# Optimization experiments

Hardware: AMD Instinct MI355X
Metric: run time of the kernel (lower is better)

## Reference

```python
import jax, jax.numpy as jnp
import numpy as np

N_EMBED = 1024
HEAD_SIZE = 128
B, T = 4, 2048

def setup_inputs() -> dict:
    key = jax.random.key(0)
    kx, kq, kk, kv = jax.random.split(key, 4)
    bound = 1.0 / np.sqrt(N_EMBED)  # torch Linear default init range
    x = jax.random.normal(kx, (B, T, N_EMBED), dtype=jnp.float32)
    Wq = jax.random.uniform(kq, (N_EMBED, HEAD_SIZE), jnp.float32, -bound, bound)
    Wk = jax.random.uniform(kk, (N_EMBED, HEAD_SIZE), jnp.float32, -bound, bound)
    Wv = jax.random.uniform(kv, (N_EMBED, HEAD_SIZE), jnp.float32, -bound, bound)
    return {"x": x, "Wq": Wq, "Wk": Wk, "Wv": Wv}

def reference(x, Wq, Wk, Wv):
    Bn, Tn, C = x.shape
    q = x @ Wq  # [B,T,H]
    k = x @ Wk
    v = x @ Wv
    # NOTE: original scales by C**-0.5 where C = n_embed (not head_size)
    scale = C ** (-0.5)
    wei = jnp.einsum('bqh,bkh->bqk', q, k) * scale  # [B,T,T]
    causal = jnp.tril(jnp.ones((Tn, Tn), dtype=bool))
    wei = jnp.where(causal, wei, -jnp.inf)
    wei = jax.nn.softmax(wei, axis=-1)
    # dropout p=0.0 -> identity
    return jnp.einsum('bqk,bkh->bqh', wei, v)
```

## Files before the change

kernel.cpp:

```cpp
#include <hip/hip_runtime.h>
#include <stdint.h>

#define B_ 4
#define T_ 2048
#define C_ 1024
#define H_ 128
#define NEG_BIG -3.0e38f

typedef __attribute__((ext_vector_type(8))) short short8;
typedef __attribute__((ext_vector_type(4))) float f32x4;
typedef __attribute__((ext_vector_type(4))) unsigned short ushort4v;
typedef __attribute__((ext_vector_type(8))) unsigned short ushort8v;

__device__ __forceinline__ unsigned short f2bf(float f) {
  union { float f; unsigned u; } cv; cv.f = f;
  unsigned u = cv.u;
  return (unsigned short)((u + 0x7fffu + ((u >> 16) & 1u)) >> 16);
}

__device__ __forceinline__ float bf2f(unsigned short s) {
  union { unsigned u; float f; } cv; cv.u = ((unsigned)s) << 16;
  return cv.f;
}

__device__ __forceinline__ void gld16(const unsigned short* g, unsigned short* l) {
  __builtin_amdgcn_global_load_lds(
      (const __attribute__((address_space(1))) unsigned int*)g,
      (__attribute__((address_space(3))) unsigned int*)l, 16, 0, 0);
}

#define CSCALE 0.045084220027780106f

__global__ __launch_bounds__(256) void prep(const float* __restrict__ x,
                                            const float* __restrict__ Wq,
                                            const float* __restrict__ Wk,
                                            const float* __restrict__ Wv,
                                            unsigned short* __restrict__ xb,
                                            unsigned short* __restrict__ WbT) {
  if (blockIdx.x < 8192) {
    const int base = (blockIdx.x * 256 + threadIdx.x) * 4;
    f32x4 v = *(const f32x4*)(x + base);
    ushort4v p;
    p[0] = f2bf(v[0]); p[1] = f2bf(v[1]); p[2] = f2bf(v[2]); p[3] = f2bf(v[3]);
    *(ushort4v*)(xb + base) = p;
  } else {
    const int i = (blockIdx.x - 8192) * 256 + threadIdx.x;
    const int linear = i * 4;
    const int j = linear >> 10;
    const int k0 = linear & 1023;
    const float* W = (j < 128) ? Wq : (j < 256) ? Wk : Wv;
    const int h = j & 127;
    ushort4v p;
    p[0] = f2bf(W[(k0 + 0) * 128 + h]);
    p[1] = f2bf(W[(k0 + 1) * 128 + h]);
    p[2] = f2bf(W[(k0 + 2) * 128 + h]);
    p[3] = f2bf(W[(k0 + 3) * 128 + h]);
    *(ushort4v*)(WbT + linear) = p;
  }
}

__global__ __launch_bounds__(256) void qkv_proj(const unsigned short* __restrict__ xb,
                                                const unsigned short* __restrict__ WbT,
                                                unsigned short* __restrict__ Qb,
                                                unsigned short* __restrict__ Kb,
                                                unsigned short* __restrict__ VT) {
  __shared__ unsigned short As[2][64 * 64];
  __shared__ unsigned short Bs[2][96 * 64];

  const int tid  = threadIdx.x;
  const int wave = tid >> 6, lane = tid & 63;
  const int quad = lane >> 4, l15 = lane & 15;
  const int rb = blockIdx.x >> 2, cb = blockIdx.x & 3;
  const int gm0 = rb * 64, gn0 = cb * 96;
  const int wm = wave >> 1, wn = wave & 1;

  const int srow = lane >> 3, sslot = lane & 7;

  int aoff[2][2], boff[3][2];
#pragma unroll
  for (int mt = 0; mt < 2; ++mt) {
    const int r = wm * 32 + mt * 16 + l15;
#pragma unroll
    for (int ks = 0; ks < 2; ++ks)
      aoff[mt][ks] = r * 64 + (((ks * 4 + quad) ^ r) & 7) * 8;
  }
#pragma unroll
  for (int nt = 0; nt < 3; ++nt) {
    const int r = wn * 48 + nt * 16 + l15;
#pragma unroll
    for (int ks = 0; ks < 2; ++ks)
      boff[nt][ks] = r * 64 + (((ks * 4 + quad) ^ r) & 7) * 8;
  }

  f32x4 acc[2][3];
  const f32x4 zero4 = {0.f, 0.f, 0.f, 0.f};
#pragma unroll
  for (int mt = 0; mt < 2; ++mt)
#pragma unroll
    for (int nt = 0; nt < 3; ++nt) acc[mt][nt] = zero4;

#define STAGE_QKV(buf, kb_)                                                        \
  {                                                                                \
    const int ko = (kb_) * 64;                                                     \
    _Pragma("unroll")                                                              \
    for (int q = 0; q < 2; ++q) {                                                  \
      const int row = wave * 16 + q * 8 + srow;                                    \
      gld16(xb + (size_t)(gm0 + row) * C_ + ko + ((sslot ^ row) & 7) * 8,          \
            &As[buf][(wave * 16 + q * 8) * 64]);                                   \
    }                                                                              \
    _Pragma("unroll")                                                              \
    for (int q = 0; q < 3; ++q) {                                                  \
      const int row = wave * 24 + q * 8 + srow;                                    \
      gld16(WbT + (size_t)(gn0 + row) * C_ + ko + ((sslot ^ row) & 7) * 8,         \
            &Bs[buf][(wave * 24 + q * 8) * 64]);                                   \
    }                                                                              \
  }

  STAGE_QKV(0, 0);

  for (int kb = 0; kb < 16; ++kb) {
    __syncthreads();
    if (kb + 1 < 16) STAGE_QKV((kb + 1) & 1, kb + 1);
    const unsigned short* Ac = As[kb & 1];
    const unsigned short* Bc = Bs[kb & 1];
#pragma unroll
    for (int ks = 0; ks < 2; ++ks) {
      short8 a0 = *(const short8*)(Ac + aoff[0][ks]);
      short8 a1 = *(const short8*)(Ac + aoff[1][ks]);
      short8 b0 = *(const short8*)(Bc + boff[0][ks]);
      short8 b1 = *(const short8*)(Bc + boff[1][ks]);
      short8 b2 = *(const short8*)(Bc + boff[2][ks]);
      acc[0][0] = __builtin_amdgcn_mfma_f32_16x16x32_bf16(a0, b0, acc[0][0], 0, 0, 0);
      acc[0][1] = __builtin_amdgcn_mfma_f32_16x16x32_bf16(a0, b1, acc[0][1], 0, 0, 0);
      acc[0][2] = __builtin_amdgcn_mfma_f32_16x16x32_bf16(a0, b2, acc[0][2], 0, 0, 0);
      acc[1][0] = __builtin_amdgcn_mfma_f32_16x16x32_bf16(a1, b0, acc[1][0], 0, 0, 0);
      acc[1][1] = __builtin_amdgcn_mfma_f32_16x16x32_bf16(a1, b1, acc[1][1], 0, 0, 0);
      acc[1][2] = __builtin_amdgcn_mfma_f32_16x16x32_bf16(a1, b2, acc[1][2], 0, 0, 0);
    }
  }
#undef STAGE_QKV

#pragma unroll
  for (int mt = 0; mt < 2; ++mt) {
    const int row0 = gm0 + wm * 32 + mt * 16 + quad * 4;
#pragma unroll
    for (int nt = 0; nt < 3; ++nt) {
      const int colbase = gn0 + wn * 48 + nt * 16;
      const int col = colbase + l15;
      if (colbase < 128) {
#pragma unroll
        for (int r = 0; r < 4; ++r)
          Qb[(size_t)(row0 + r) * H_ + col] = f2bf(acc[mt][nt][r] * CSCALE);
      } else if (colbase < 256) {
#pragma unroll
        for (int r = 0; r < 4; ++r)
          Kb[(size_t)(row0 + r) * H_ + (col - 128)] = f2bf(acc[mt][nt][r]);
      } else {
        const int h = col - 256;
        const int bidx = row0 >> 11;
        const int t0 = row0 & 2047;
        ushort4v pk;
        pk[0] = f2bf(acc[mt][nt][0]); pk[1] = f2bf(acc[mt][nt][1]);
        pk[2] = f2bf(acc[mt][nt][2]); pk[3] = f2bf(acc[mt][nt][3]);
        *(ushort4v*)(VT + (size_t)(bidx * H_ + h) * T_ + t0) = pk;
      }
    }
  }
}

__global__ __launch_bounds__(256, 2) void attn1(const unsigned short* __restrict__ Qb,
                                                const unsigned short* __restrict__ Kb,
                                                const unsigned short* __restrict__ VT,
                                                unsigned short* __restrict__ Opart,
                                                float* __restrict__ mpart,
                                                float* __restrict__ lpart,
                                                float* __restrict__ out) {
  __shared__ unsigned short Ks[2][64 * 128];
  __shared__ unsigned short Vs[2][128 * 64];
  __shared__ unsigned short Pls[4][16 * 72];
  __shared__ float Als[4][16];

  const int bid = blockIdx.x;
  const int b  = bid & 3;
  const int j  = (bid >> 2) & 31;
  const int ch = bid >> 7;
  if (ch * 4 > j) return;
  const int ntiles = min(4, j + 1 - ch * 4);

  const int tid  = threadIdx.x;
  const int wave = tid >> 6, lane = tid & 63;
  const int quad = lane >> 4, l15 = lane & 15;

  const unsigned short* qrow = Qb + (size_t)(b * T_ + j * 64 + wave * 16 + l15) * H_;
  short8 aq[4];
#pragma unroll
  for (int ks = 0; ks < 4; ++ks)
    aq[ks] = *(const short8*)(qrow + ks * 32 + quad * 8);

  const unsigned short* Kb_b = Kb + (size_t)(b * T_) * H_;
  const unsigned short* VT_b = VT + (size_t)(b * H_) * T_;

  const int k_row4 = lane >> 4, k_slot = lane & 15;
  const int v_row8 = lane >> 3, v_slot = lane & 7;

#define STAGE_KV(buf, kv0_)                                                        \
  {                                                                                \
    _Pragma("unroll")                                                              \
    for (int i = 0; i < 4; ++i) {                                                  \
      const int r = wave * 16 + i * 4 + k_row4;                                    \
      const int c2 = (k_slot & 8) | ((k_slot ^ r) & 7);                            \
      gld16(Kb_b + (size_t)((kv0_) + r) * H_ + c2 * 8,                             \
            &Ks[buf][(wave * 16 + i * 4) * 128]);                                  \
    }                                                                              \
    _Pragma("unroll")                                                              \
    for (int i = 0; i < 4; ++i) {                                                  \
      const int h = wave * 32 + i * 8 + v_row8;                                    \
      gld16(VT_b + (size_t)h * T_ + (kv0_) + ((v_slot ^ h) & 7) * 8,               \
            &Vs[buf][(wave * 32 + i * 8) * 64]);                                   \
    }                                                                              \
  }

  STAGE_KV(0, ch * 256);

  const f32x4 zero4 = {0.f, 0.f, 0.f, 0.f};
  f32x4 O[8];
#pragma unroll
  for (int nth = 0; nth < 8; ++nth) O[nth] = zero4;
  float m_ = NEG_BIG, l_ = 0.f;

  for (int t = 0; t < ntiles; ++t) {
    __syncthreads();
    const int kv0 = ch * 256 + t * 64;
    if (t + 1 < ntiles) STAGE_KV((t + 1) & 1, kv0 + 64);

    const unsigned short* kb = Ks[t & 1];
    f32x4 ST[4];
    ST[0] = zero4; ST[1] = zero4; ST[2] = zero4; ST[3] = zero4;
#pragma unroll
    for (int ntl = 0; ntl < 4; ++ntl) {
      const int kvr = ntl * 16 + l15;
#pragma unroll
      for (int ks = 0; ks < 4; ++ks) {
        const int c = ks * 4 + quad;
        const int slot = (c & 8) | ((c ^ kvr) & 7);
        short8 kf = *(const short8*)(kb + kvr * 128 + slot * 8);
        ST[ntl] = __builtin_amdgcn_mfma_f32_16x16x32_bf16(kf, aq[ks], ST[ntl], 0, 0, 0);
      }
    }

    if (ch * 4 + t == j) {
      const int ql = j * 64 + wave * 16 + l15;
#pragma unroll
      for (int ntl = 0; ntl < 4; ++ntl)
#pragma unroll
        for (int r = 0; r < 4; ++r) {
          const int kl = kv0 + ntl * 16 + quad * 4 + r;
          if (kl > ql) ST[ntl][r] = NEG_BIG;
        }
    }

    float vmax = ST[0][0];
#pragma unroll
    for (int ntl = 0; ntl < 4; ++ntl)
#pragma unroll
      for (int r = 0; r < 4; ++r) vmax = fmaxf(vmax, ST[ntl][r]);
    vmax = fmaxf(vmax, __shfl_xor(vmax, 16));
    vmax = fmaxf(vmax, __shfl_xor(vmax, 32));
    const float mn = fmaxf(m_, vmax);
    const float alpha = __builtin_amdgcn_exp2f(m_ - mn);
    m_ = mn;
    float s = 0.f;
#pragma unroll
    for (int ntl = 0; ntl < 4; ++ntl)
#pragma unroll
      for (int r = 0; r < 4; ++r) {
        const float p = __builtin_amdgcn_exp2f(ST[ntl][r] - mn);
        ST[ntl][r] = p;
        s += p;
      }
    s += __shfl_xor(s, 16);
    s += __shfl_xor(s, 32);
    l_ = l_ * alpha + s;

#pragma unroll
    for (int ntl = 0; ntl < 4; ++ntl) {
      ushort4v pk;
      pk[0] = f2bf(ST[ntl][0]); pk[1] = f2bf(ST[ntl][1]);
      pk[2] = f2bf(ST[ntl][2]); pk[3] = f2bf(ST[ntl][3]);
      *(ushort4v*)(&Pls[wave][l15 * 72 + ntl * 16 + quad * 4]) = pk;
    }

    if (lane < 16) Als[wave][lane] = alpha;
    if (!__all(alpha == 1.f)) {
      f32x4 al4 = *(const f32x4*)&Als[wave][quad * 4];
#pragma unroll
      for (int nth = 0; nth < 8; ++nth)
#pragma unroll
        for (int r = 0; r < 4; ++r) O[nth][r] *= al4[r];
    }

    const unsigned short* vb = Vs[t & 1];
    short8 ap0 = *(const short8*)(&Pls[wave][l15 * 72 + quad * 8]);
    short8 ap1 = *(const short8*)(&Pls[wave][l15 * 72 + 32 + quad * 8]);
#pragma unroll
    for (int nth = 0; nth < 8; ++nth) {
      const int h = nth * 16 + l15;
      short8 v0 = *(const short8*)(vb + h * 64 + ((quad ^ h) & 7) * 8);
      short8 v1 = *(const short8*)(vb + h * 64 + (((4 + quad) ^ h) & 7) * 8);
      O[nth] = __builtin_amdgcn_mfma_f32_16x16x32_bf16(ap0, v0, O[nth], 0, 0, 0);
      O[nth] = __builtin_amdgcn_mfma_f32_16x16x32_bf16(ap1, v1, O[nth], 0, 0, 0);
    }
  }
#undef STAGE_KV

  if ((j >> 2) == 0) {
    if (lane < 16) Als[wave][lane] = 1.0f / l_;
    f32x4 li4 = *(const f32x4*)&Als[wave][quad * 4];
    float* op = out + (size_t)(b * T_ + j * 64 + wave * 16) * H_;
#pragma unroll
    for (int nth = 0; nth < 8; ++nth)
#pragma unroll
      for (int r = 0; r < 4; ++r)
        op[(quad * 4 + r) * H_ + nth * 16 + l15] = O[nth][r] * li4[r];
  } else {
    const int pid = (b * 32 + j) * 8 + ch;
    unsigned short* po = Opart + (size_t)(pid * 64 + wave * 16) * H_;
#pragma unroll
    for (int nth = 0; nth < 8; ++nth)
#pragma unroll
      for (int r = 0; r < 4; ++r)
        po[(quad * 4 + r) * H_ + nth * 16 + l15] = f2bf(O[nth][r]);
    if (lane < 16) {
      mpart[pid * 64 + wave * 16 + lane] = m_;
      lpart[pid * 64 + wave * 16 + lane] = l_;
    }
  }
}

__global__ __launch_bounds__(256) void attn2(const unsigned short* __restrict__ Opart,
                                             const float* __restrict__ mpart,
                                             const float* __restrict__ lpart,
                                             float* __restrict__ out) {
  const int b = blockIdx.x & 3;
  const int j = 4 + (blockIdx.x >> 2);
  const int nch = (j >> 2) + 1;
  const int tid = threadIdx.x;
  const int qh = tid >> 4;
  const int h0 = (tid & 15) * 8;
  const int pbase = (b * 32 + j) * 8;

#pragma unroll
  for (int i = 0; i < 4; ++i) {
    const int q = qh + i * 16;
    float m_fin = NEG_BIG;
    for (int ch = 0; ch < nch; ++ch)
      m_fin = fmaxf(m_fin, mpart[(pbase + ch) * 64 + q]);
    float lf = 0.f;
    float o[8];
#pragma unroll
    for (int c = 0; c < 8; ++c) o[c] = 0.f;
    for (int ch = 0; ch < nch; ++ch) {
      const int pid = pbase + ch;
      const float sc = __builtin_amdgcn_exp2f(mpart[pid * 64 + q] - m_fin);
      lf += sc * lpart[pid * 64 + q];
      ushort8v pv = *(const ushort8v*)(Opart + (size_t)(pid * 64 + q) * H_ + h0);
#pragma unroll
      for (int c = 0; c < 8; ++c) o[c] += sc * bf2f(pv[c]);
    }
    const float inv = 1.0f / lf;
    float* op = out + (size_t)(b * T_ + j * 64 + q) * H_ + h0;
    f32x4 v0 = {o[0] * inv, o[1] * inv, o[2] * inv, o[3] * inv};
    f32x4 v1 = {o[4] * inv, o[5] * inv, o[6] * inv, o[7] * inv};
    *(f32x4*)(op) = v0;
    *(f32x4*)(op + 4) = v1;
  }
}

extern "C" void kernel_launch(void* const* d_in, const int* in_sizes, int n_in,
                              void* d_out, int out_size, void* d_ws, size_t ws_size,
                              hipStream_t stream) {
  const float* x  = (const float*)d_in[0];
  const float* Wq = (const float*)d_in[1];
  const float* Wk = (const float*)d_in[2];
  const float* Wv = (const float*)d_in[3];
  float* out = (float*)d_out;

  char* ws = (char*)d_ws;
  unsigned short* xb  = (unsigned short*)(ws);
  unsigned short* WbT = (unsigned short*)(ws + 16777216);
  unsigned short* Qb  = (unsigned short*)(ws + 17563648);
  unsigned short* Kb  = (unsigned short*)(ws + 19660800);
  unsigned short* VT  = (unsigned short*)(ws + 21757952);
  unsigned short* Opart = (unsigned short*)(ws);
  float* mpart = (float*)(ws + 16777216);
  float* lpart = (float*)(ws + 17039360);

  prep<<<dim3(8576), dim3(256), 0, stream>>>(x, Wq, Wk, Wv, xb, WbT);
  qkv_proj<<<dim3(512), dim3(256), 0, stream>>>(xb, WbT, Qb, Kb, VT);
  attn1<<<dim3(1024), dim3(256), 0, stream>>>(Qb, Kb, VT, Opart, mpart, lpart, out);
  attn2<<<dim3(112), dim3(256), 0, stream>>>(Opart, mpart, lpart, out);
}
```

Measured before the change: 141.7 us.

## Fuse x fp32-to-bf16 conversion into QKV projection load path

Result: slower. 151.5 us (+6.9%).

```diff
diff --git a/kernel.cpp b/kernel.cpp
--- a/kernel.cpp
+++ b/kernel.cpp
@@ -14,8 +14,7 @@
 
 __device__ __forceinline__ unsigned short f2bf(float f) {
   union { float f; unsigned u; } cv; cv.f = f;
-  unsigned u = cv.u;
-  return (unsigned short)((u + 0x7fffu + ((u >> 16) & 1u)) >> 16);
+  return (unsigned short)((cv.u + 0x8000u) >> 16);
 }
 
 __device__ __forceinline__ float bf2f(unsigned short s) {
@@ -23,7 +22,7 @@
   return cv.f;
 }
 
-__device__ __forceinline__ void gld16(const unsigned short* g, unsigned short* l) {
+__device__ __forceinline__ void gld16(const void* g, void* l) {
   __builtin_amdgcn_global_load_lds(
       (const __attribute__((address_space(1))) unsigned int*)g,
       (__attribute__((address_space(3))) unsigned int*)l, 16, 0, 0);
@@ -31,40 +30,30 @@
 
 #define CSCALE 0.045084220027780106f
 
-__global__ __launch_bounds__(256) void prep(const float* __restrict__ x,
-                                            const float* __restrict__ Wq,
-                                            const float* __restrict__ Wk,
-                                            const float* __restrict__ Wv,
-                                            unsigned short* __restrict__ xb,
-                                            unsigned short* __restrict__ WbT) {
-  if (blockIdx.x < 8192) {
-    const int base = (blockIdx.x * 256 + threadIdx.x) * 4;
-    f32x4 v = *(const f32x4*)(x + base);
-    ushort4v p;
-    p[0] = f2bf(v[0]); p[1] = f2bf(v[1]); p[2] = f2bf(v[2]); p[3] = f2bf(v[3]);
-    *(ushort4v*)(xb + base) = p;
-  } else {
-    const int i = (blockIdx.x - 8192) * 256 + threadIdx.x;
-    const int linear = i * 4;
-    const int j = linear >> 10;
-    const int k0 = linear & 1023;
-    const float* W = (j < 128) ? Wq : (j < 256) ? Wk : Wv;
-    const int h = j & 127;
-    ushort4v p;
-    p[0] = f2bf(W[(k0 + 0) * 128 + h]);
-    p[1] = f2bf(W[(k0 + 1) * 128 + h]);
-    p[2] = f2bf(W[(k0 + 2) * 128 + h]);
-    p[3] = f2bf(W[(k0 + 3) * 128 + h]);
-    *(ushort4v*)(WbT + linear) = p;
-  }
-}
-
-__global__ __launch_bounds__(256) void qkv_proj(const unsigned short* __restrict__ xb,
+__global__ __launch_bounds__(256) void prep_w(const float* __restrict__ Wq,
+                                              const float* __restrict__ Wk,
+                                              const float* __restrict__ Wv,
+                                              unsigned short* __restrict__ WbT) {
+  const int i = blockIdx.x * 256 + threadIdx.x;
+  const int linear = i * 4;
+  const int j = linear >> 10;
+  const int k0 = linear & 1023;
+  const float* W = (j < 128) ? Wq : (j < 256) ? Wk : Wv;
+  const int h = j & 127;
+  ushort4v p;
+  p[0] = f2bf(W[(k0 + 0) * 128 + h]);
+  p[1] = f2bf(W[(k0 + 1) * 128 + h]);
+  p[2] = f2bf(W[(k0 + 2) * 128 + h]);
+  p[3] = f2bf(W[(k0 + 3) * 128 + h]);
+  *(ushort4v*)(WbT + linear) = p;
+}
+
+__global__ __launch_bounds__(256) void qkv_proj(const float* __restrict__ x,
                                                 const unsigned short* __restrict__ WbT,
                                                 unsigned short* __restrict__ Qb,
                                                 unsigned short* __restrict__ Kb,
                                                 unsigned short* __restrict__ VT) {
-  __shared__ unsigned short As[2][64 * 64];
+  __shared__ float          Asf[2][64 * 64];
   __shared__ unsigned short Bs[2][96 * 64];
 
   const int tid  = threadIdx.x;
@@ -74,22 +63,30 @@
   const int gm0 = rb * 64, gn0 = cb * 96;
   const int wm = wave >> 1, wn = wave & 1;
 
-  const int srow = lane >> 3, sslot = lane & 7;
-
-  int aoff[2][2], boff[3][2];
-#pragma unroll
-  for (int mt = 0; mt < 2; ++mt) {
-    const int r = wm * 32 + mt * 16 + l15;
-#pragma unroll
-    for (int ks = 0; ks < 2; ++ks)
-      aoff[mt][ks] = r * 64 + (((ks * 4 + quad) ^ r) & 7) * 8;
-  }
+  const int a_row4 = lane >> 4, a_slot = lane & 15;
+  const int b_row8 = lane >> 3, b_slot = lane & 7;
+
+  int boff[3][2];
 #pragma unroll
   for (int nt = 0; nt < 3; ++nt) {
     const int r = wn * 48 + nt * 16 + l15;
 #pragma unroll
     for (int ks = 0; ks < 2; ++ks)
       boff[nt][ks] = r * 64 + (((ks * 4 + quad) ^ r) & 7) * 8;
+  }
+  int aoff[2][2][2];
+#pragma unroll
+  for (int mt = 0; mt < 2; ++mt) {
+    const int m = wm * 32 + mt * 16 + l15;
+#pragma unroll
+    for (int ks = 0; ks < 2; ++ks) {
+      const int c0 = ks * 8 + quad * 2;
+      const int s0 = (c0 & 8) | ((c0 ^ m) & 7);
+      const int c1 = c0 + 1;
+      const int s1 = (c1 & 8) | ((c1 ^ m) & 7);
+      aoff[mt][ks][0] = m * 64 + s0 * 4;
+      aoff[mt][ks][1] = m * 64 + s1 * 4;
+    }
   }
 
   f32x4 acc[2][3];
@@ -103,15 +100,16 @@
   {                                                                                \
     const int ko = (kb_) * 64;                                                     \
     _Pragma("unroll")                                                              \
-    for (int q = 0; q < 2; ++q) {                                                  \
-      const int row = wave * 16 + q * 8 + srow;                                    \
-      gld16(xb + (size_t)(gm0 + row) * C_ + ko + ((sslot ^ row) & 7) * 8,          \
-            &As[buf][(wave * 16 + q * 8) * 64]);                                   \
+    for (int q = 0; q < 4; ++q) {                                                  \
+      const int row = wave * 16 + q * 4 + a_row4;                                  \
+      const int c = (a_slot & 8) | ((a_slot ^ row) & 7);                           \
+      gld16(x + (size_t)(gm0 + row) * C_ + ko + c * 4,                             \
+            &Asf[buf][(wave * 16 + q * 4) * 64]);                                  \
     }                                                                              \
     _Pragma("unroll")                                                              \
     for (int q = 0; q < 3; ++q) {                                                  \
-      const int row = wave * 24 + q * 8 + srow;                                    \
-      gld16(WbT + (size_t)(gn0 + row) * C_ + ko + ((sslot ^ row) & 7) * 8,         \
+      const int row = wave * 24 + q * 8 + b_row8;                                  \
+      gld16(WbT + (size_t)(gn0 + row) * C_ + ko + ((b_slot ^ row) & 7) * 8,        \
             &Bs[buf][(wave * 24 + q * 8) * 64]);                                   \
     }                                                                              \
   }
@@ -121,21 +119,30 @@
   for (int kb = 0; kb < 16; ++kb) {
     __syncthreads();
     if (kb + 1 < 16) STAGE_QKV((kb + 1) & 1, kb + 1);
-    const unsigned short* Ac = As[kb & 1];
+    const float* Ac = Asf[kb & 1];
     const unsigned short* Bc = Bs[kb & 1];
 #pragma unroll
     for (int ks = 0; ks < 2; ++ks) {
-      short8 a0 = *(const short8*)(Ac + aoff[0][ks]);
-      short8 a1 = *(const short8*)(Ac + aoff[1][ks]);
+      short8 a[2];
+#pragma unroll
+      for (int mt = 0; mt < 2; ++mt) {
+        f32x4 va = *(const f32x4*)(Ac + aoff[mt][ks][0]);
+        f32x4 vb = *(const f32x4*)(Ac + aoff[mt][ks][1]);
+#pragma unroll
+        for (int e = 0; e < 4; ++e) {
+          a[mt][e]     = (short)f2bf(va[e]);
+          a[mt][4 + e] = (short)f2bf(vb[e]);
+        }
+      }
       short8 b0 = *(const short8*)(Bc + boff[0][ks]);
       short8 b1 = *(const short8*)(Bc + boff[1][ks]);
       short8 b2 = *(const short8*)(Bc + boff[2][ks]);
-      acc[0][0] = __builtin_amdgcn_mfma_f32_16x16x32_bf16(a0, b0, acc[0][0], 0, 0, 0);
-      acc[0][1] = __builtin_amdgcn_mfma_f32_16x16x32_bf16(a0, b1, acc[0][1], 0, 0, 0);
-      acc[0][2] = __builtin_amdgcn_mfma_f32_16x16x32_bf16(a0, b2, acc[0][2], 0, 0, 0);
-      acc[1][0] = __builtin_amdgcn_mfma_f32_16x16x32_bf16(a1, b0, acc[1][0], 0, 0, 0);
-      acc[1][1] = __builtin_amdgcn_mfma_f32_16x16x32_bf16(a1, b1, acc[1][1], 0, 0, 0);
-      acc[1][2] = __builtin_amdgcn_mfma_f32_16x16x32_bf16(a1, b2, acc[1][2], 0, 0, 0);
+      acc[0][0] = __builtin_amdgcn_mfma_f32_16x16x32_bf16(a[0], b0, acc[0][0], 0, 0, 0);
+      acc[0][1] = __builtin_amdgcn_mfma_f32_16x16x32_bf16(a[0], b1, acc[0][1], 0, 0, 0);
+      acc[0][2] = __builtin_amdgcn_mfma_f32_16x16x32_bf16(a[0], b2, acc[0][2], 0, 0, 0);
+      acc[1][0] = __builtin_amdgcn_mfma_f32_16x16x32_bf16(a[1], b0, acc[1][0], 0, 0, 0);
+      acc[1][1] = __builtin_amdgcn_mfma_f32_16x16x32_bf16(a[1], b1, acc[1][1], 0, 0, 0);
+      acc[1][2] = __builtin_amdgcn_mfma_f32_16x16x32_bf16(a[1], b2, acc[1][2], 0, 0, 0);
     }
   }
 #undef STAGE_QKV
@@ -386,17 +393,16 @@
   float* out = (float*)d_out;
 
   char* ws = (char*)d_ws;
-  unsigned short* xb  = (unsigned short*)(ws);
-  unsigned short* WbT = (unsigned short*)(ws + 16777216);
-  unsigned short* Qb  = (unsigned short*)(ws + 17563648);
-  unsigned short* Kb  = (unsigned short*)(ws + 19660800);
-  unsigned short* VT  = (unsigned short*)(ws + 21757952);
-  unsigned short* Opart = (unsigned short*)(ws);
-  float* mpart = (float*)(ws + 16777216);
-  float* lpart = (float*)(ws + 17039360);
-
-  prep<<<dim3(8576), dim3(256), 0, stream>>>(x, Wq, Wk, Wv, xb, WbT);
-  qkv_proj<<<dim3(512), dim3(256), 0, stream>>>(xb, WbT, Qb, Kb, VT);
+  unsigned short* WbT = (unsigned short*)(ws);
+  unsigned short* Qb  = (unsigned short*)(ws + 1048576);
+  unsigned short* Kb  = (unsigned short*)(ws + 3145728);
+  unsigned short* VT  = (unsigned short*)(ws + 5242880);
+  unsigned short* Opart = (unsigned short*)(ws + 8388608);
+  float* mpart = (float*)(ws + 25165824);
+  float* lpart = (float*)(ws + 25427968);
+
+  prep_w<<<dim3(384), dim3(256), 0, stream>>>(Wq, Wk, Wv, WbT);
+  qkv_proj<<<dim3(512), dim3(256), 0, stream>>>(x, WbT, Qb, Kb, VT);
   attn1<<<dim3(1024), dim3(256), 0, stream>>>(Qb, Kb, VT, Opart, mpart, lpart, out);
   attn2<<<dim3(112), dim3(256), 0, stream>>>(Opart, mpart, lpart, out);
 }
```

## Fuse split-KV combine into attention kernel via last-block atomic counter

Applied to the files above, without the earlier changes.

Measured after the change: 233.8 us. 1.65x slower.

```diff
diff --git a/kernel.cpp b/kernel.cpp
--- a/kernel.cpp
+++ b/kernel.cpp
@@ -14,8 +14,7 @@
 
 __device__ __forceinline__ unsigned short f2bf(float f) {
   union { float f; unsigned u; } cv; cv.f = f;
-  unsigned u = cv.u;
-  return (unsigned short)((u + 0x7fffu + ((u >> 16) & 1u)) >> 16);
+  return (unsigned short)((cv.u + 0x8000u) >> 16);
 }
 
 __device__ __forceinline__ float bf2f(unsigned short s) {
@@ -23,7 +22,7 @@
   return cv.f;
 }
 
-__device__ __forceinline__ void gld16(const unsigned short* g, unsigned short* l) {
+__device__ __forceinline__ void gld16(const void* g, void* l) {
   __builtin_amdgcn_global_load_lds(
       (const __attribute__((address_space(1))) unsigned int*)g,
       (__attribute__((address_space(3))) unsigned int*)l, 16, 0, 0);
@@ -36,14 +35,15 @@
                                             const float* __restrict__ Wk,
                                             const float* __restrict__ Wv,
                                             unsigned short* __restrict__ xb,
-                                            unsigned short* __restrict__ WbT) {
+                                            unsigned short* __restrict__ WbT,
+                                            int* __restrict__ counters) {
   if (blockIdx.x < 8192) {
     const int base = (blockIdx.x * 256 + threadIdx.x) * 4;
     f32x4 v = *(const f32x4*)(x + base);
     ushort4v p;
     p[0] = f2bf(v[0]); p[1] = f2bf(v[1]); p[2] = f2bf(v[2]); p[3] = f2bf(v[3]);
     *(ushort4v*)(xb + base) = p;
-  } else {
+  } else if (blockIdx.x < 8576) {
     const int i = (blockIdx.x - 8192) * 256 + threadIdx.x;
     const int linear = i * 4;
     const int j = linear >> 10;
@@ -56,6 +56,8 @@
     p[2] = f2bf(W[(k0 + 2) * 128 + h]);
     p[3] = f2bf(W[(k0 + 3) * 128 + h]);
     *(ushort4v*)(WbT + linear) = p;
+  } else {
+    if (threadIdx.x < 128) counters[threadIdx.x] = 0;
   }
 }
 
@@ -174,11 +176,13 @@
                                                 unsigned short* __restrict__ Opart,
                                                 float* __restrict__ mpart,
                                                 float* __restrict__ lpart,
+                                                int* __restrict__ counters,
                                                 float* __restrict__ out) {
   __shared__ unsigned short Ks[2][64 * 128];
   __shared__ unsigned short Vs[2][128 * 64];
   __shared__ unsigned short Pls[4][16 * 72];
   __shared__ float Als[4][16];
+  __shared__ int lastf;
 
   const int bid = blockIdx.x;
   const int b  = bid & 3;
@@ -334,45 +338,45 @@
       mpart[pid * 64 + wave * 16 + lane] = m_;
       lpart[pid * 64 + wave * 16 + lane] = l_;
     }
-  }
-}
-
-__global__ __launch_bounds__(256) void attn2(const unsigned short* __restrict__ Opart,
-                                             const float* __restrict__ mpart,
-                                             const float* __restrict__ lpart,
-                                             float* __restrict__ out) {
-  const int b = blockIdx.x & 3;
-  const int j = 4 + (blockIdx.x >> 2);
-  const int nch = (j >> 2) + 1;
-  const int tid = threadIdx.x;
-  const int qh = tid >> 4;
-  const int h0 = (tid & 15) * 8;
-  const int pbase = (b * 32 + j) * 8;
-
-#pragma unroll
-  for (int i = 0; i < 4; ++i) {
-    const int q = qh + i * 16;
-    float m_fin = NEG_BIG;
-    for (int ch = 0; ch < nch; ++ch)
-      m_fin = fmaxf(m_fin, mpart[(pbase + ch) * 64 + q]);
-    float lf = 0.f;
-    float o[8];
-#pragma unroll
-    for (int c = 0; c < 8; ++c) o[c] = 0.f;
-    for (int ch = 0; ch < nch; ++ch) {
-      const int pid = pbase + ch;
-      const float sc = __builtin_amdgcn_exp2f(mpart[pid * 64 + q] - m_fin);
-      lf += sc * lpart[pid * 64 + q];
-      ushort8v pv = *(const ushort8v*)(Opart + (size_t)(pid * 64 + q) * H_ + h0);
-#pragma unroll
-      for (int c = 0; c < 8; ++c) o[c] += sc * bf2f(pv[c]);
-    }
-    const float inv = 1.0f / lf;
-    float* op = out + (size_t)(b * T_ + j * 64 + q) * H_ + h0;
-    f32x4 v0 = {o[0] * inv, o[1] * inv, o[2] * inv, o[3] * inv};
-    f32x4 v1 = {o[4] * inv, o[5] * inv, o[6] * inv, o[7] * inv};
-    *(f32x4*)(op) = v0;
-    *(f32x4*)(op + 4) = v1;
+
+    const int nch = (j >> 2) + 1;
+    __threadfence();
+    if (tid == 0) {
+      const int old = atomicAdd(&counters[b * 32 + j], 1);
+      lastf = (old == nch - 1);
+    }
+    __syncthreads();
+    if (lastf) {
+      __threadfence();
+      const int pbase = (b * 32 + j) * 8;
+      const int qh = tid >> 4;
+      const int h0 = (tid & 15) * 8;
+#pragma unroll
+      for (int i = 0; i < 4; ++i) {
+        const int q = qh + i * 16;
+        float m_fin = NEG_BIG;
+        for (int c2 = 0; c2 < nch; ++c2)
+          m_fin = fmaxf(m_fin, mpart[(pbase + c2) * 64 + q]);
+        float lf = 0.f;
+        float o[8];
+#pragma unroll
+        for (int c = 0; c < 8; ++c) o[c] = 0.f;
+        for (int c2 = 0; c2 < nch; ++c2) {
+          const int pid2 = pbase + c2;
+          const float sc = __builtin_amdgcn_exp2f(mpart[pid2 * 64 + q] - m_fin);
+          lf += sc * lpart[pid2 * 64 + q];
+          ushort8v pv = *(const ushort8v*)(Opart + (size_t)(pid2 * 64 + q) * H_ + h0);
+#pragma unroll
+          for (int c = 0; c < 8; ++c) o[c] += sc * bf2f(pv[c]);
+        }
+        const float inv = 1.0f / lf;
+        float* op = out + (size_t)(b * T_ + j * 64 + q) * H_ + h0;
+        f32x4 v0 = {o[0] * inv, o[1] * inv, o[2] * inv, o[3] * inv};
+        f32x4 v1 = {o[4] * inv, o[5] * inv, o[6] * inv, o[7] * inv};
+        *(f32x4*)(op) = v0;
+        *(f32x4*)(op + 4) = v1;
+      }
+    }
   }
 }
 
@@ -394,9 +398,10 @@
   unsigned short* Opart = (unsigned short*)(ws);
   float* mpart = (float*)(ws + 16777216);
   float* lpart = (float*)(ws + 17039360);
-
-  prep<<<dim3(8576), dim3(256), 0, stream>>>(x, Wq, Wk, Wv, xb, WbT);
+  int* counters = (int*)(ws + 25165824);
+
+  prep<<<dim3(8577), dim3(256), 0, stream>>>(x, Wq, Wk, Wv, xb, WbT, counters);
   qkv_proj<<<dim3(512), dim3(256), 0, stream>>>(xb, WbT, Qb, Kb, VT);
-  attn1<<<dim3(1024), dim3(256), 0, stream>>>(Qb, Kb, VT, Opart, mpart, lpart, out);
-  attn2<<<dim3(112), dim3(256), 0, stream>>>(Opart, mpart, lpart, out);
-}
+  attn1<<<dim3(1024), dim3(256), 0, stream>>>(Qb, Kb, VT, Opart, mpart, lpart,
+                                              counters, out);
+}
```

## Fuse x bf16 conversion into QKV projection and retile to 32x192 blocks

Applied to the files above, without the earlier changes.

After: 142.6 us. Within noise of the previous version (+0.6%).

```diff
diff --git a/kernel.cpp b/kernel.cpp
--- a/kernel.cpp
+++ b/kernel.cpp
@@ -14,8 +14,7 @@
 
 __device__ __forceinline__ unsigned short f2bf(float f) {
   union { float f; unsigned u; } cv; cv.f = f;
-  unsigned u = cv.u;
-  return (unsigned short)((u + 0x7fffu + ((u >> 16) & 1u)) >> 16);
+  return (unsigned short)((cv.u + 0x8000u) >> 16);
 }
 
 __device__ __forceinline__ float bf2f(unsigned short s) {
@@ -23,7 +22,7 @@
   return cv.f;
 }
 
-__device__ __forceinline__ void gld16(const unsigned short* g, unsigned short* l) {
+__device__ __forceinline__ void gld16(const void* g, void* l) {
   __builtin_amdgcn_global_load_lds(
       (const __attribute__((address_space(1))) unsigned int*)g,
       (__attribute__((address_space(3))) unsigned int*)l, 16, 0, 0);
@@ -31,62 +30,56 @@
 
 #define CSCALE 0.045084220027780106f
 
-__global__ __launch_bounds__(256) void prep(const float* __restrict__ x,
-                                            const float* __restrict__ Wq,
-                                            const float* __restrict__ Wk,
-                                            const float* __restrict__ Wv,
-                                            unsigned short* __restrict__ xb,
-                                            unsigned short* __restrict__ WbT) {
-  if (blockIdx.x < 8192) {
-    const int base = (blockIdx.x * 256 + threadIdx.x) * 4;
-    f32x4 v = *(const f32x4*)(x + base);
-    ushort4v p;
-    p[0] = f2bf(v[0]); p[1] = f2bf(v[1]); p[2] = f2bf(v[2]); p[3] = f2bf(v[3]);
-    *(ushort4v*)(xb + base) = p;
-  } else {
-    const int i = (blockIdx.x - 8192) * 256 + threadIdx.x;
-    const int linear = i * 4;
-    const int j = linear >> 10;
-    const int k0 = linear & 1023;
-    const float* W = (j < 128) ? Wq : (j < 256) ? Wk : Wv;
-    const int h = j & 127;
-    ushort4v p;
-    p[0] = f2bf(W[(k0 + 0) * 128 + h]);
-    p[1] = f2bf(W[(k0 + 1) * 128 + h]);
-    p[2] = f2bf(W[(k0 + 2) * 128 + h]);
-    p[3] = f2bf(W[(k0 + 3) * 128 + h]);
-    *(ushort4v*)(WbT + linear) = p;
-  }
-}
-
-__global__ __launch_bounds__(256) void qkv_proj(const unsigned short* __restrict__ xb,
+__global__ __launch_bounds__(256) void prep_w(const float* __restrict__ Wq,
+                                              const float* __restrict__ Wk,
+                                              const float* __restrict__ Wv,
+                                              unsigned short* __restrict__ WbT) {
+  const int i = blockIdx.x * 256 + threadIdx.x;
+  const int linear = i * 4;
+  const int j = linear >> 10;
+  const int k0 = linear & 1023;
+  const float* W = (j < 128) ? Wq : (j < 256) ? Wk : Wv;
+  const int h = j & 127;
+  ushort4v p;
+  p[0] = f2bf(W[(k0 + 0) * 128 + h]);
+  p[1] = f2bf(W[(k0 + 1) * 128 + h]);
+  p[2] = f2bf(W[(k0 + 2) * 128 + h]);
+  p[3] = f2bf(W[(k0 + 3) * 128 + h]);
+  *(ushort4v*)(WbT + linear) = p;
+}
+
+__global__ __launch_bounds__(256) void qkv_proj(const float* __restrict__ x,
                                                 const unsigned short* __restrict__ WbT,
                                                 unsigned short* __restrict__ Qb,
                                                 unsigned short* __restrict__ Kb,
                                                 unsigned short* __restrict__ VT) {
-  __shared__ unsigned short As[2][64 * 64];
-  __shared__ unsigned short Bs[2][96 * 64];
+  __shared__ unsigned short As[2][32 * 64];
+  __shared__ unsigned short Bs[2][192 * 64];
 
   const int tid  = threadIdx.x;
   const int wave = tid >> 6, lane = tid & 63;
   const int quad = lane >> 4, l15 = lane & 15;
-  const int rb = blockIdx.x >> 2, cb = blockIdx.x & 3;
-  const int gm0 = rb * 64, gn0 = cb * 96;
-  const int wm = wave >> 1, wn = wave & 1;
+  const int rb = blockIdx.x >> 1, cb = blockIdx.x & 1;
+  const int gm0 = rb * 32, gn0 = cb * 192;
+
+  const int ar = tid >> 3, ac = tid & 7;
+  const float* gA = x + (size_t)(gm0 + ar) * C_ + ac * 8;
+  unsigned short* lA = (unsigned short*)&As[0][0] + ar * 64 + ((ac ^ ar) & 7) * 8;
+  const int lAstride = 32 * 64;
 
   const int srow = lane >> 3, sslot = lane & 7;
 
   int aoff[2][2], boff[3][2];
 #pragma unroll
   for (int mt = 0; mt < 2; ++mt) {
-    const int r = wm * 32 + mt * 16 + l15;
+    const int r = mt * 16 + l15;
 #pragma unroll
     for (int ks = 0; ks < 2; ++ks)
       aoff[mt][ks] = r * 64 + (((ks * 4 + quad) ^ r) & 7) * 8;
   }
 #pragma unroll
   for (int nt = 0; nt < 3; ++nt) {
-    const int r = wn * 48 + nt * 16 + l15;
+    const int r = wave * 48 + nt * 16 + l15;
 #pragma unroll
     for (int ks = 0; ks < 2; ++ks)
       boff[nt][ks] = r * 64 + (((ks * 4 + quad) ^ r) & 7) * 8;
@@ -99,30 +92,42 @@
 #pragma unroll
     for (int nt = 0; nt < 3; ++nt) acc[mt][nt] = zero4;
 
-#define STAGE_QKV(buf, kb_)                                                        \
+#define STAGE_B(buf, kb_)                                                          \
   {                                                                                \
     const int ko = (kb_) * 64;                                                     \
     _Pragma("unroll")                                                              \
-    for (int q = 0; q < 2; ++q) {                                                  \
-      const int row = wave * 16 + q * 8 + srow;                                    \
-      gld16(xb + (size_t)(gm0 + row) * C_ + ko + ((sslot ^ row) & 7) * 8,          \
-            &As[buf][(wave * 16 + q * 8) * 64]);                                   \
+    for (int q = 0; q < 6; ++q) {                                                  \
+      const int row = wave * 48 + q * 8 + srow;                                    \
+      gld16(WbT + (size_t)(gn0 + row) * C_ + ko + ((sslot ^ row) & 7) * 8,         \
+            &Bs[buf][(wave * 48 + q * 8) * 64]);                                   \
     }                                                                              \
-    _Pragma("unroll")                                                              \
-    for (int q = 0; q < 3; ++q) {                                                  \
-      const int row = wave * 24 + q * 8 + srow;                                    \
-      gld16(WbT + (size_t)(gn0 + row) * C_ + ko + ((sslot ^ row) & 7) * 8,         \
-            &Bs[buf][(wave * 24 + q * 8) * 64]);                                   \
-    }                                                                              \
-  }
-
-  STAGE_QKV(0, 0);
+  }
+
+  {
+    f32x4 va = *(const f32x4*)(gA);
+    f32x4 vb = *(const f32x4*)(gA + 4);
+    STAGE_B(0, 0);
+    short8 aw;
+#pragma unroll
+    for (int e = 0; e < 4; ++e) {
+      aw[e]     = (short)f2bf(va[e]);
+      aw[4 + e] = (short)f2bf(vb[e]);
+    }
+    *(short8*)lA = aw;
+  }
 
   for (int kb = 0; kb < 16; ++kb) {
     __syncthreads();
-    if (kb + 1 < 16) STAGE_QKV((kb + 1) & 1, kb + 1);
-    const unsigned short* Ac = As[kb & 1];
-    const unsigned short* Bc = Bs[kb & 1];
+    const int cur = kb & 1, nxt = cur ^ 1;
+    f32x4 va, vb;
+    if (kb + 1 < 16) {
+      const int ko = (kb + 1) * 64;
+      va = *(const f32x4*)(gA + ko);
+      vb = *(const f32x4*)(gA + ko + 4);
+      STAGE_B(nxt, kb + 1);
+    }
+    const unsigned short* Ac = As[cur];
+    const unsigned short* Bc = Bs[cur];
 #pragma unroll
     for (int ks = 0; ks < 2; ++ks) {
       short8 a0 = *(const short8*)(Ac + aoff[0][ks]);
@@ -137,15 +142,24 @@
       acc[1][1] = __builtin_amdgcn_mfma_f32_16x16x32_bf16(a1, b1, acc[1][1], 0, 0, 0);
       acc[1][2] = __builtin_amdgcn_mfma_f32_16x16x32_bf16(a1, b2, acc[1][2], 0, 0, 0);
     }
-  }
-#undef STAGE_QKV
+    if (kb + 1 < 16) {
+      short8 aw;
+#pragma unroll
+      for (int e = 0; e < 4; ++e) {
+        aw[e]     = (short)f2bf(va[e]);
+        aw[4 + e] = (short)f2bf(vb[e]);
+      }
+      *(short8*)(lA + nxt * lAstride) = aw;
+    }
+  }
+#undef STAGE_B
 
 #pragma unroll
   for (int mt = 0; mt < 2; ++mt) {
-    const int row0 = gm0 + wm * 32 + mt * 16 + quad * 4;
+    const int row0 = gm0 + mt * 16 + quad * 4;
 #pragma unroll
     for (int nt = 0; nt < 3; ++nt) {
-      const int colbase = gn0 + wn * 48 + nt * 16;
+      const int colbase = gn0 + wave * 48 + nt * 16;
       const int col = colbase + l15;
       if (colbase < 128) {
 #pragma unroll
@@ -386,17 +400,16 @@
   float* out = (float*)d_out;
 
   char* ws = (char*)d_ws;
-  unsigned short* xb  = (unsigned short*)(ws);
-  unsigned short* WbT = (unsigned short*)(ws + 16777216);
-  unsigned short* Qb  = (unsigned short*)(ws + 17563648);
-  unsigned short* Kb  = (unsigned short*)(ws + 19660800);
-  unsigned short* VT  = (unsigned short*)(ws + 21757952);
   unsigned short* Opart = (unsigned short*)(ws);
   float* mpart = (float*)(ws + 16777216);
   float* lpart = (float*)(ws + 17039360);
-
-  prep<<<dim3(8576), dim3(256), 0, stream>>>(x, Wq, Wk, Wv, xb, WbT);
-  qkv_proj<<<dim3(512), dim3(256), 0, stream>>>(xb, WbT, Qb, Kb, VT);
+  unsigned short* WbT = (unsigned short*)(ws + 17563648);
+  unsigned short* Qb  = (unsigned short*)(ws + 18350080);
+  unsigned short* Kb  = (unsigned short*)(ws + 20447232);
+  unsigned short* VT  = (unsigned short*)(ws + 22544384);
+
+  prep_w<<<dim3(384), dim3(256), 0, stream>>>(Wq, Wk, Wv, WbT);
+  qkv_proj<<<dim3(512), dim3(256), 0, stream>>>(x, WbT, Qb, Kb, VT);
   attn1<<<dim3(1024), dim3(256), 0, stream>>>(Qb, Kb, VT, Opart, mpart, lpart, out);
   attn2<<<dim3(112), dim3(256), 0, stream>>>(Opart, mpart, lpart, out);
 }
```
